# Optimization experiments

Hardware: AMD Instinct MI355X
Metric: run time of the kernel (lower is better)

## Reference

```python
import jax, jax.numpy as jnp
import numpy as np

B, S, D_MODEL, D_ATTN = 4, 2048, 1024, 1024
NEG_INF = jnp.float32(-jnp.inf)


def setup_inputs() -> dict:
    key = jax.random.key(0)
    ks = jax.random.split(key, 6)
    scale = 1.0 / np.sqrt(D_MODEL)
    return {
        "x": jax.random.normal(ks[0], (B, S, D_MODEL), dtype=jnp.float32),
        "mask": jnp.ones((B, S), dtype=jnp.float32),
        "Wq": jax.random.normal(ks[1], (D_ATTN, D_MODEL), dtype=jnp.float32) * scale,
        "Wk": jax.random.normal(ks[2], (D_ATTN, D_MODEL), dtype=jnp.float32) * scale,
        "Wv": jax.random.normal(ks[3], (D_ATTN, D_MODEL), dtype=jnp.float32) * scale,
        "Wo": jax.random.normal(ks[4], (D_MODEL, D_ATTN), dtype=jnp.float32) * scale,
        "bo": jnp.zeros((D_MODEL,), dtype=jnp.float32),
    }


def reference(x, mask, Wq, Wk, Wv, Wo, bo):
    # x: [B,S,Dm]; torch Linear weight is [out,in], so y = x @ W.T
    q = jnp.einsum("bsd,ad->bsa", x, Wq)  # [B,S,Da]
    k = jnp.einsum("bsd,ad->bsa", x, Wk)
    v = jnp.einsum("bsd,ad->bsa", x, Wv)  # NOTE: v from x (original quirk)
    logits = jnp.einsum("bqa,bka->bqk", q, k)  # [B,S,S]
    # causal mask (cross_attention=True path): keep lower triangle incl. diag
    causal = jnp.tril(jnp.ones((S, S), dtype=bool))
    logits = jnp.where(causal[None], logits, NEG_INF)
    # padding mask: outer product of per-token mask
    square_mask = mask[:, :, None] * mask[:, None, :]  # [B,S,S]
    logits = jnp.where(square_mask == 1, logits, NEG_INF)
    # scale by sqrt(d_model) AFTER masking (as in original)
    attn = jax.nn.softmax(logits / jnp.sqrt(jnp.float32(D_MODEL)), axis=-1)
    attn_out = jnp.einsum("bqk,bka->bqa", attn, v)  # [B,S,Da]
    return jnp.einsum("bsa,da->bsd", attn_out, Wo) + bo
```

## Files before the change

### kernel.cpp

```cpp
#include <hip/hip_runtime.h>
#include <hip/hip_bf16.h>
#include <cstdio>

typedef __bf16 bf16x8 __attribute__((ext_vector_type(8)));
typedef float f32x4 __attribute__((ext_vector_type(4)));

#define BM 128
#define BN 128
#define BK 64

__device__ __forceinline__ unsigned short f2bf(float f) {
  union { float f; unsigned u; } v; v.f = f;
  unsigned u = v.u;
  return (unsigned short)((u + 0x7FFFu + ((u >> 16) & 1u)) >> 16);
}

__device__ __forceinline__ float bf2f(unsigned short s) {
  union { unsigned u; float f; } v; v.u = ((unsigned)s) << 16;
  return v.f;
}

#define GLOAD16(gsrc, ldst) \
  __builtin_amdgcn_global_load_lds((const __attribute__((address_space(1))) void*)(gsrc), \
                                   (__attribute__((address_space(3))) void*)(ldst), 16, 0, 0)

#define SB_KLOOP(Ab, Bb)                                                        \
  for (int kt = 0; kt < 16; kt++) {                                             \
    const unsigned short* Ak = (Ab) + kt * BK;                                  \
    const unsigned short* Bk = (Bb) + kt * BK;                                  \
    _Pragma("unroll")                                                           \
    for (int r = 0; r < 4; r++) {                                               \
      int row = r * 32 + srow;                                                  \
      int sc = sch ^ (row & 7);                                                 \
      GLOAD16(Ak + (long)row * 1024 + sc * 8, &lds[0][(r * 32 + wave * 8) * BK]);\
    }                                                                           \
    _Pragma("unroll")                                                           \
    for (int r = 0; r < 4; r++) {                                               \
      int row = r * 32 + srow;                                                  \
      int sc = sch ^ (row & 7);                                                 \
      GLOAD16(Bk + (long)row * 1024 + sc * 8, &lds[1][(r * 32 + wave * 8) * BK]);\
    }                                                                           \
    __syncthreads();                                                            \
    _Pragma("unroll")                                                           \
    for (int s = 0; s < 2; s++) {                                               \
      bf16x8 av[4], bv[4];                                                      \
      _Pragma("unroll")                                                         \
      for (int i = 0; i < 4; i++) av[i] = *reinterpret_cast<const bf16x8*>(lds[0] + aOff[i][s]); \
      _Pragma("unroll")                                                         \
      for (int j = 0; j < 4; j++) bv[j] = *reinterpret_cast<const bf16x8*>(lds[1] + bOff[j][s]); \
      _Pragma("unroll")                                                         \
      for (int i = 0; i < 4; i++)                                               \
        _Pragma("unroll")                                                       \
        for (int j = 0; j < 4; j++)                                             \
          acc[i][j] = __builtin_amdgcn_mfma_f32_16x16x32_bf16(av[i], bv[j], acc[i][j], 0, 0, 0); \
    }                                                                           \
    __syncthreads();                                                            \
  }

#define SB_PREAMBLE                                                             \
  const int tid = threadIdx.x;                                                  \
  const int lane = tid & 63;                                                    \
  const int wave = tid >> 6;                                                    \
  const int wr = wave >> 1, wc = wave & 1;                                      \
  const int srow = tid >> 3;                                                    \
  const int sch = tid & 7;                                                      \
  const f32x4 fzero = {0.f, 0.f, 0.f, 0.f};                                     \
  f32x4 acc[4][4];                                                              \
  _Pragma("unroll")                                                             \
  for (int i = 0; i < 4; i++)                                                   \
    _Pragma("unroll")                                                           \
    for (int j = 0; j < 4; j++) acc[i][j] = fzero;                              \
  int aOff[4][2], bOff[4][2];                                                   \
  _Pragma("unroll")                                                             \
  for (int i = 0; i < 4; i++) {                                                 \
    _Pragma("unroll")                                                           \
    for (int s = 0; s < 2; s++) {                                               \
      int ra = wr * 64 + i * 16 + (lane & 15);                                  \
      aOff[i][s] = ra * BK + (((s * 4 + (lane >> 4)) ^ (ra & 7)) * 8);          \
      int rb = wc * 64 + i * 16 + (lane & 15);                                  \
      bOff[i][s] = rb * BK + (((s * 4 + (lane >> 4)) ^ (rb & 7)) * 8);          \
    }                                                                           \
  }

__global__ __launch_bounds__(256)
void cast_w(const float* __restrict__ Wq, const float* __restrict__ Wk,
            const float* __restrict__ Wv, const float* __restrict__ Wo,
            unsigned short* __restrict__ Wqk, unsigned short* __restrict__ Wob,
            unsigned short* __restrict__ Wvt)
{
  const int blk = blockIdx.x;
  const int tid = threadIdx.x;
  if (blk < 1536) {
    const int w = blk >> 9;
    const int off = blk & 511;
    const float* src = (w == 0) ? Wq : (w == 1) ? Wk : Wo;
    unsigned short* dst = (w == 0) ? Wqk : (w == 1) ? (Wqk + 1024L * 1024) : Wob;
    const int i = (off * 256 + tid) * 8;
    float4 a = *reinterpret_cast<const float4*>(src + i);
    float4 b = *reinterpret_cast<const float4*>(src + i + 4);
    union { unsigned short us[8]; uint4 u4; } pk;
    pk.us[0] = f2bf(a.x); pk.us[1] = f2bf(a.y); pk.us[2] = f2bf(a.z); pk.us[3] = f2bf(a.w);
    pk.us[4] = f2bf(b.x); pk.us[5] = f2bf(b.y); pk.us[6] = f2bf(b.z); pk.us[7] = f2bf(b.w);
    *reinterpret_cast<uint4*>(dst + i) = pk.u4;
    return;
  }
  __shared__ float t[64][65];
  const int tile = blk - 1536;
  const int a0 = (tile >> 4) * 64;
  const int m0 = (tile & 15) * 64;
#pragma unroll
  for (int i = 0; i < 4; i++) {
    const int row = (tid >> 4) + i * 16;
    const int col4 = tid & 15;
    float4 f4 = *reinterpret_cast<const float4*>(Wv + (long)(a0 + row) * 1024 + m0 + col4 * 4);
    t[row][col4 * 4 + 0] = f4.x;
    t[row][col4 * 4 + 1] = f4.y;
    t[row][col4 * 4 + 2] = f4.z;
    t[row][col4 * 4 + 3] = f4.w;
  }
  __syncthreads();
#pragma unroll
  for (int j = 0; j < 2; j++) {
    const int mm = (tid >> 3) + j * 32;
    const int aa0 = (tid & 7) * 8;
    union { unsigned short us[8]; uint4 u4; } pk;
#pragma unroll
    for (int u = 0; u < 8; u++) pk.us[u] = f2bf(t[aa0 + u][mm]);
    *reinterpret_cast<uint4*>(Wvt + (long)(m0 + mm) * 1024 + a0 + aa0) = pk.u4;
  }
}

__global__ __launch_bounds__(256, 3)
void prep2(const float* __restrict__ x, unsigned short* __restrict__ xb,
           const unsigned short* __restrict__ Wob, const unsigned short* __restrict__ Wvt,
           unsigned short* __restrict__ Wvo)
{
  __shared__ short lds[2][BM * BK];
  if (blockIdx.x >= 64) {
    const int blk = blockIdx.x - 64;
    const int i = (blk * 256 + (int)threadIdx.x) * 8;
    float4 a = *reinterpret_cast<const float4*>(x + i);
    float4 b = *reinterpret_cast<const float4*>(x + i + 4);
    union { unsigned short us[8]; uint4 u4; } pk;
    pk.us[0] = f2bf(a.x); pk.us[1] = f2bf(a.y); pk.us[2] = f2bf(a.z); pk.us[3] = f2bf(a.w);
    pk.us[4] = f2bf(b.x); pk.us[5] = f2bf(b.y); pk.us[6] = f2bf(b.z); pk.us[7] = f2bf(b.w);
    *reinterpret_cast<uint4*>(xb + i) = pk.u4;
    return;
  }
  const int t = blockIdx.x;
  const int m0 = (t >> 3) * BM, n0 = (t & 7) * BN;
  const unsigned short* Ab = Wob + (long)m0 * 1024;
  const unsigned short* Bb = Wvt + (long)n0 * 1024;

  SB_PREAMBLE
  SB_KLOOP(Ab, Bb)

  const int rb4 = (lane >> 4) * 4;
  const int cl = lane & 15;
#pragma unroll
  for (int i = 0; i < 4; i++) {
#pragma unroll
    for (int j = 0; j < 4; j++) {
      const int gm = m0 + wr * 64 + i * 16 + rb4;
      const int gn = n0 + wc * 64 + j * 16 + cl;
#pragma unroll
      for (int r = 0; r < 4; r++)
        Wvo[(long)(gm + r) * 1024 + gn] = f2bf(acc[i][j][r]);
    }
  }
}

__global__ __launch_bounds__(256, 3)
void dispA2(const unsigned short* __restrict__ Xbf, const unsigned short* __restrict__ Wqk,
            const unsigned short* __restrict__ Wvo,
            unsigned short* __restrict__ Qb, unsigned short* __restrict__ Kb,
            unsigned short* __restrict__ VWt)
{
  __shared__ short lds[2][BM * BK];
  const int flat = blockIdx.x;
  const bool isQK = flat < 1024;
  int m0, n0;
  const unsigned short *Ab, *Bb;
  if (isQK) {
    const int swz = (flat & 7) * 128 + (flat >> 3);
    const int bx = swz & 15, by = swz >> 4;
    m0 = by * BM; n0 = bx * BN;
    Ab = Xbf + (long)m0 * 1024;
    Bb = Wqk + (long)n0 * 1024;
  } else {
    const int t = flat - 1024;
    const int swz = (t & 7) * 64 + (t >> 3);
    const int bx = swz & 7, by = swz >> 3;
    m0 = by * BM; n0 = bx * BN;
    Ab = Xbf + (long)m0 * 1024;
    Bb = Wvo + (long)n0 * 1024;
  }

  SB_PREAMBLE
  SB_KLOOP(Ab, Bb)

  const int rb4 = (lane >> 4) * 4;
  const int cl = lane & 15;
#pragma unroll
  for (int i = 0; i < 4; i++) {
#pragma unroll
    for (int j = 0; j < 4; j++) {
      const int gm = m0 + wr * 64 + i * 16 + rb4;
      const int gn = n0 + wc * 64 + j * 16 + cl;
      if (isQK) {
        if (gn < 1024) {
#pragma unroll
          for (int r = 0; r < 4; r++)
            Qb[(long)(gm + r) * 1024 + gn] = f2bf(acc[i][j][r]);
        } else {
#pragma unroll
          for (int r = 0; r < 4; r++)
            Kb[(long)(gm + r) * 1024 + (gn - 1024)] = f2bf(acc[i][j][r]);
        }
      } else {
        const int b = gm >> 11;
        const int sIdx = gm & 2047;
        unsigned short* C = VWt + (long)b * (2048L * 1024) + (long)gn * 2048 + sIdx;
        ushort4 pk;
        pk.x = f2bf(acc[i][j][0]);
        pk.y = f2bf(acc[i][j][1]);
        pk.z = f2bf(acc[i][j][2]);
        pk.w = f2bf(acc[i][j][3]);
        *reinterpret_cast<ushort4*>(C) = pk;
      }
    }
  }
}

__global__ __launch_bounds__(256, 3)
void dispS(const unsigned short* __restrict__ Qb, const unsigned short* __restrict__ Kb,
           unsigned short* __restrict__ Sb)
{
  __shared__ short lds[2][BM * BK];
  const int t = blockIdx.x;
  const int bz = t / 136;
  const int tt = t - bz * 136;
  const int swz = (tt & 7) * 17 + (tt >> 3);
  int i = (int)((sqrtf(8.f * (float)swz + 1.f) - 1.f) * 0.5f);
  while ((i + 1) * (i + 2) / 2 <= swz) ++i;
  while (i * (i + 1) / 2 > swz) --i;
  const int j = swz - i * (i + 1) / 2;
  const int m0 = i * BM, n0 = j * BN;
  const unsigned short* Ab = Qb + ((long)bz * 2048 + m0) * 1024;
  const unsigned short* Bb = Kb + ((long)bz * 2048 + n0) * 1024;

  SB_PREAMBLE
  SB_KLOOP(Ab, Bb)

  const int rb4 = (lane >> 4) * 4;
  const int cl = lane & 15;
  unsigned short* C = Sb + (long)bz * (2048L * 2048);
#pragma unroll
  for (int ii = 0; ii < 4; ii++) {
#pragma unroll
    for (int jj = 0; jj < 4; jj++) {
      const int gm = m0 + wr * 64 + ii * 16 + rb4;
      const int gn = n0 + wc * 64 + jj * 16 + cl;
#pragma unroll
      for (int r = 0; r < 4; r++)
        C[(long)(gm + r) * 2048 + gn] = f2bf(acc[ii][jj][r] * 0.03125f);
    }
  }
}

__global__ __launch_bounds__(256, 2)
void gemm_pv(const unsigned short* __restrict__ A, const unsigned short* __restrict__ B,
             float* __restrict__ Cv, const float* __restrict__ bias,
             int K, int ldA, int ldB, int ldC,
             long aBat, long bBat, long cBat)
{
  const int gx = gridDim.x;
  const int nwg = gx * gridDim.y;
  const int flat = blockIdx.y * gx + blockIdx.x;
  const int qch = nwg >> 3, rch = nwg & 7;
  const int xcd = flat & 7, idx = flat >> 3;
  const int swz = (xcd < rch ? xcd * (qch + 1) : rch * (qch + 1) + (xcd - rch) * qch) + idx;
  const int bx = swz % gx;
  const int bz = blockIdx.z;
  int by = swz / gx;
  if (bz >= 2) by = gridDim.y - 1 - by;

  const int m0 = by * BM;
  const int n0 = bx * BN;

  const unsigned short* Ab = A + (long)bz * aBat + (long)m0 * ldA;
  const unsigned short* Bb = B + (long)bz * bBat + (long)n0 * ldB;

  __shared__ short lds[2][2][BM * BK];

  const int tid = threadIdx.x;
  const int lane = tid & 63;
  const int wave = tid >> 6;
  const int wr = wave >> 1, wc = wave & 1;

  const int Keff = min(K, m0 + BM);
  const int nk = Keff / BK;

  const int srow = tid >> 3;
  const int sch = tid & 7;

  const f32x4 fzero = {0.f, 0.f, 0.f, 0.f};
  f32x4 acc[4][4];
#pragma unroll
  for (int i = 0; i < 4; i++)
#pragma unroll
    for (int j = 0; j < 4; j++) acc[i][j] = fzero;

  int aOff[4][2], bOff[4][2];
#pragma unroll
  for (int i = 0; i < 4; i++) {
#pragma unroll
    for (int s = 0; s < 2; s++) {
      int ra = wr * 64 + i * 16 + (lane & 15);
      aOff[i][s] = ra * BK + (((s * 4 + (lane >> 4)) ^ (ra & 7)) * 8);
      int rb = wc * 64 + i * 16 + (lane & 15);
      bOff[i][s] = rb * BK + (((s * 4 + (lane >> 4)) ^ (rb & 7)) * 8);
    }
  }

  auto stage = [&](int buf, int kt) {
    const unsigned short* Ak = Ab + kt * BK;
    const unsigned short* Bk = Bb + kt * BK;
#pragma unroll
    for (int r = 0; r < 4; r++) {
      int row = r * 32 + srow;
      int sc = sch ^ (row & 7);
      GLOAD16(Ak + (long)row * ldA + sc * 8, &lds[buf][0][(r * 32 + wave * 8) * BK]);
    }
#pragma unroll
    for (int r = 0; r < 4; r++) {
      int row = r * 32 + srow;
      int sc = sch ^ (row & 7);
      GLOAD16(Bk + (long)row * ldB + sc * 8, &lds[buf][1][(r * 32 + wave * 8) * BK]);
    }
  };

  stage(0, 0);
  stage(1, 1);
  asm volatile("s_waitcnt vmcnt(8)" ::: "memory");
  __builtin_amdgcn_sched_barrier(0);
  __builtin_amdgcn_s_barrier();

  int cur = 0;
  for (int kt = 0; kt < nk; kt++) {
    const short* La = lds[cur][0];
    const short* Lb = lds[cur][1];
    bf16x8 av[2][4], bv[2][4];
#pragma unroll
    for (int s = 0; s < 2; s++) {
#pragma unroll
      for (int i = 0; i < 4; i++) {
        av[s][i] = *reinterpret_cast<const bf16x8*>(La + aOff[i][s]);
        bv[s][i] = *reinterpret_cast<const bf16x8*>(Lb + bOff[i][s]);
      }
    }
    asm volatile("s_waitcnt lgkmcnt(0)" ::: "memory");
    __builtin_amdgcn_sched_barrier(0);
    __builtin_amdgcn_s_barrier();
    __builtin_amdgcn_sched_barrier(0);

    if (kt + 2 < nk) {
      stage(cur, kt + 2);
      asm volatile("s_waitcnt vmcnt(8)" ::: "memory");
    } else if (kt + 1 < nk) {
      asm volatile("s_waitcnt vmcnt(0)" ::: "memory");
    }
    if (kt + 1 < nk) {
      __builtin_amdgcn_s_barrier();
      __builtin_amdgcn_sched_barrier(0);
    }

    __builtin_amdgcn_s_setprio(1);
#pragma unroll
    for (int s = 0; s < 2; s++)
#pragma unroll
      for (int i = 0; i < 4; i++)
#pragma unroll
        for (int j = 0; j < 4; j++)
          acc[i][j] = __builtin_amdgcn_mfma_f32_16x16x32_bf16(av[s][i], bv[s][j], acc[i][j], 0, 0, 0);
    __builtin_amdgcn_s_setprio(0);
    __builtin_amdgcn_sched_barrier(0);
    cur ^= 1;
  }

  const int rb4 = (lane >> 4) * 4;
  const int cl = lane & 15;
#pragma unroll
  for (int i = 0; i < 4; i++) {
#pragma unroll
    for (int j = 0; j < 4; j++) {
      const int gm = m0 + wr * 64 + i * 16 + rb4;
      const int gn = n0 + wc * 64 + j * 16 + cl;
      float* C = Cv + (long)bz * cBat;
      const float bb = bias[gn];
#pragma unroll
      for (int r = 0; r < 4; r++)
        C[(long)(gm + r) * ldC + gn] = acc[i][j][r] + bb;
    }
  }
}

__global__ __launch_bounds__(256)
void softmax_rows(const unsigned short* __restrict__ Sb, const float* __restrict__ maskv,
                  unsigned short* __restrict__ P, int Sdim)
{
  const int wv = threadIdx.x >> 6;
  const int lane = threadIdx.x & 63;
  const int q = blockIdx.x * 4 + wv;
  const int b = blockIdx.y;
  const int kmax = (q & ~127) + 128;
  const unsigned short* row = Sb + ((long)b * Sdim + q) * Sdim;
  unsigned short* prow = P + ((long)b * Sdim + q) * Sdim;
  const float* mrow = maskv + (long)b * Sdim;
  const float mq = mrow[q];

  float v[4][8];
  float mx = -INFINITY;
#pragma unroll
  for (int c = 0; c < 4; c++) {
    const int k0 = c * 512 + lane * 8;
    if (c * 512 < kmax) {
      uint4 raw = *reinterpret_cast<const uint4*>(row + k0);
      const unsigned short* us = reinterpret_cast<const unsigned short*>(&raw);
      float4 ma = *reinterpret_cast<const float4*>(mrow + k0);
      float4 mb = *reinterpret_cast<const float4*>(mrow + k0 + 4);
      float mv[8] = {ma.x, ma.y, ma.z, ma.w, mb.x, mb.y, mb.z, mb.w};
#pragma unroll
      for (int u = 0; u < 8; u++) {
        const int k = k0 + u;
        const bool ok = (k <= q) && (mq * mv[u] == 1.0f);
        v[c][u] = ok ? bf2f(us[u]) : -INFINITY;
        mx = fmaxf(mx, v[c][u]);
      }
    } else {
#pragma unroll
      for (int u = 0; u < 8; u++) v[c][u] = -INFINITY;
    }
  }
#pragma unroll
  for (int o = 32; o; o >>= 1) mx = fmaxf(mx, __shfl_xor(mx, o));

  float sm = 0.f;
#pragma unroll
  for (int c = 0; c < 4; c++)
#pragma unroll
    for (int u = 0; u < 8; u++) {
      v[c][u] = (v[c][u] > -INFINITY) ? __expf(v[c][u] - mx) : 0.f;
      sm += v[c][u];
    }
#pragma unroll
  for (int o = 32; o; o >>= 1) sm += __shfl_xor(sm, o);
  const float inv = 1.0f / sm;

#pragma unroll
  for (int c = 0; c < 4; c++) {
    if (c * 512 < kmax) {
      union { unsigned short us[8]; uint4 u4; } pk;
#pragma unroll
      for (int u = 0; u < 8; u++) pk.us[u] = f2bf(v[c][u] * inv);
      *reinterpret_cast<uint4*>(prow + c * 512 + lane * 8) = pk.u4;
    }
  }
}

extern "C" void kernel_launch(void* const* d_in, const int* in_sizes, int n_in,
                              void* d_out, int out_size, void* d_ws, size_t ws_size,
                              hipStream_t stream)
{
  const int B = 4, S = 2048, D = 1024;
  const float* x  = (const float*)d_in[0];
  const float* mk = (const float*)d_in[1];
  const float* Wq = (const float*)d_in[2];
  const float* Wk = (const float*)d_in[3];
  const float* Wv = (const float*)d_in[4];
  const float* Wo = (const float*)d_in[5];
  const float* bo = (const float*)d_in[6];
  float* out = (float*)d_out;

  char* ws = (char*)d_ws;
  const long MB = 1024L * 1024L;
  unsigned short* Xbf  = (unsigned short*)(ws + 0);
  unsigned short* Qb   = (unsigned short*)(ws + 16 * MB);
  unsigned short* Kb   = (unsigned short*)(ws + 32 * MB);
  unsigned short* VWt  = (unsigned short*)(ws + 48 * MB);
  unsigned short* Wqk  = (unsigned short*)(ws + 64 * MB);
  unsigned short* Wvo  = (unsigned short*)(ws + 68 * MB);
  unsigned short* Wob  = (unsigned short*)(ws + 70 * MB);
  unsigned short* Sbuf = (unsigned short*)(ws + 72 * MB);
  unsigned short* Wvt  = Sbuf;
  unsigned short* P    = Qb;

  if (ws_size < (size_t)(104 * MB)) {
    fprintf(stderr, "kernel_launch: ws too small (%zu bytes, need 104MB)\n", ws_size);
    return;
  }

  cast_w<<<dim3(1792), dim3(256), 0, stream>>>(Wq, Wk, Wv, Wo, Wqk, Wob, Wvt);
  prep2<<<dim3(4160), dim3(256), 0, stream>>>(x, Xbf, Wob, Wvt, Wvo);
  dispA2<<<dim3(1536), dim3(256), 0, stream>>>(Xbf, Wqk, Wvo, Qb, Kb, VWt);
  dispS<<<dim3(544), dim3(256), 0, stream>>>(Qb, Kb, Sbuf);
  softmax_rows<<<dim3(512, 4), dim3(256), 0, stream>>>(Sbuf, mk, P, 2048);
  dim3 gO(1024 / BN, 2048 / BM, 4);
  gemm_pv<<<gO, dim3(256), 0, stream>>>(P, VWt, out, bo,
                                        2048, 2048, 2048, 1024,
                                        (long)S * S, (long)D * S, (long)S * D);
}
```

Measured before the change: 155.7 us.

## Fuse weight casting and Wo·Wv product into one prep kernel

```diff
diff --git a/kernel.cpp b/kernel.cpp
--- a/kernel.cpp
+++ b/kernel.cpp
@@ -64,6 +64,7 @@
   const int wr = wave >> 1, wc = wave & 1;                                      \
   const int srow = tid >> 3;                                                    \
   const int sch = tid & 7;                                                      \
+  (void)srow; (void)sch;                                                        \
   const f32x4 fzero = {0.f, 0.f, 0.f, 0.f};                                     \
   f32x4 acc[4][4];                                                              \
   _Pragma("unroll")                                                             \
@@ -82,20 +83,30 @@
     }                                                                           \
   }
 
-__global__ __launch_bounds__(256)
-void cast_w(const float* __restrict__ Wq, const float* __restrict__ Wk,
-            const float* __restrict__ Wv, const float* __restrict__ Wo,
-            unsigned short* __restrict__ Wqk, unsigned short* __restrict__ Wob,
-            unsigned short* __restrict__ Wvt)
+__global__ __launch_bounds__(256, 3)
+void prep_all(const float* __restrict__ x, const float* __restrict__ Wq,
+              const float* __restrict__ Wk, const float* __restrict__ Wv,
+              const float* __restrict__ Wo,
+              unsigned short* __restrict__ xb, unsigned short* __restrict__ Wqk,
+              unsigned short* __restrict__ Wvo)
 {
+  __shared__ short lds[2][BM * BK];
   const int blk = blockIdx.x;
-  const int tid = threadIdx.x;
-  if (blk < 1536) {
-    const int w = blk >> 9;
-    const int off = blk & 511;
-    const float* src = (w == 0) ? Wq : (w == 1) ? Wk : Wo;
-    unsigned short* dst = (w == 0) ? Wqk : (w == 1) ? (Wqk + 1024L * 1024) : Wob;
-    const int i = (off * 256 + tid) * 8;
+
+  if (blk >= 64) {
+    const int tid = threadIdx.x;
+    const float* src;
+    unsigned short* dst;
+    int i;
+    if (blk < 4160) {
+      src = x; dst = xb; i = ((blk - 64) * 256 + tid) * 8;
+    } else {
+      const int w = (blk - 4160) >> 9;
+      const int off = (blk - 4160) & 511;
+      src = (w == 0) ? Wq : Wk;
+      dst = Wqk + (long)w * 1024 * 1024;
+      i = (off * 256 + tid) * 8;
+    }
     float4 a = *reinterpret_cast<const float4*>(src + i);
     float4 b = *reinterpret_cast<const float4*>(src + i + 4);
     union { unsigned short us[8]; uint4 u4; } pk;
@@ -104,56 +115,57 @@
     *reinterpret_cast<uint4*>(dst + i) = pk.u4;
     return;
   }
-  __shared__ float t[64][65];
-  const int tile = blk - 1536;
-  const int a0 = (tile >> 4) * 64;
-  const int m0 = (tile & 15) * 64;
-#pragma unroll
-  for (int i = 0; i < 4; i++) {
-    const int row = (tid >> 4) + i * 16;
-    const int col4 = tid & 15;
-    float4 f4 = *reinterpret_cast<const float4*>(Wv + (long)(a0 + row) * 1024 + m0 + col4 * 4);
-    t[row][col4 * 4 + 0] = f4.x;
-    t[row][col4 * 4 + 1] = f4.y;
-    t[row][col4 * 4 + 2] = f4.z;
-    t[row][col4 * 4 + 3] = f4.w;
-  }
-  __syncthreads();
-#pragma unroll
-  for (int j = 0; j < 2; j++) {
-    const int mm = (tid >> 3) + j * 32;
-    const int aa0 = (tid & 7) * 8;
-    union { unsigned short us[8]; uint4 u4; } pk;
-#pragma unroll
-    for (int u = 0; u < 8; u++) pk.us[u] = f2bf(t[aa0 + u][mm]);
-    *reinterpret_cast<uint4*>(Wvt + (long)(m0 + mm) * 1024 + a0 + aa0) = pk.u4;
-  }
-}
-
-__global__ __launch_bounds__(256, 3)
-void prep2(const float* __restrict__ x, unsigned short* __restrict__ xb,
-           const unsigned short* __restrict__ Wob, const unsigned short* __restrict__ Wvt,
-           unsigned short* __restrict__ Wvo)
-{
-  __shared__ short lds[2][BM * BK];
-  if (blockIdx.x >= 64) {
-    const int blk = blockIdx.x - 64;
-    const int i = (blk * 256 + (int)threadIdx.x) * 8;
-    float4 a = *reinterpret_cast<const float4*>(x + i);
-    float4 b = *reinterpret_cast<const float4*>(x + i + 4);
-    union { unsigned short us[8]; uint4 u4; } pk;
-    pk.us[0] = f2bf(a.x); pk.us[1] = f2bf(a.y); pk.us[2] = f2bf(a.z); pk.us[3] = f2bf(a.w);
-    pk.us[4] = f2bf(b.x); pk.us[5] = f2bf(b.y); pk.us[6] = f2bf(b.z); pk.us[7] = f2bf(b.w);
-    *reinterpret_cast<uint4*>(xb + i) = pk.u4;
-    return;
-  }
-  const int t = blockIdx.x;
-  const int m0 = (t >> 3) * BM, n0 = (t & 7) * BN;
-  const unsigned short* Ab = Wob + (long)m0 * 1024;
-  const unsigned short* Bb = Wvt + (long)n0 * 1024;
+
+  const int m0 = (blk >> 3) * BM, n0 = (blk & 7) * BN;
 
   SB_PREAMBLE
-  SB_KLOOP(Ab, Bb)
+
+  for (int kt = 0; kt < 16; kt++) {
+#pragma unroll
+    for (int p = 0; p < 4; p++) {
+      const int row = p * 32 + (tid >> 3);
+      const int oct = tid & 7;
+      const float* src = Wo + (long)(m0 + row) * 1024 + kt * 64 + oct * 8;
+      float4 a = *reinterpret_cast<const float4*>(src);
+      float4 b = *reinterpret_cast<const float4*>(src + 4);
+      union { unsigned short us[8]; uint4 u4; } pk;
+      pk.us[0] = f2bf(a.x); pk.us[1] = f2bf(a.y); pk.us[2] = f2bf(a.z); pk.us[3] = f2bf(a.w);
+      pk.us[4] = f2bf(b.x); pk.us[5] = f2bf(b.y); pk.us[6] = f2bf(b.z); pk.us[7] = f2bf(b.w);
+      *reinterpret_cast<uint4*>(&lds[0][row * 64 + ((oct ^ (row & 7)) * 8)]) = pk.u4;
+    }
+    {
+      const int kl = tid >> 2;
+      const int nq = tid & 3;
+      const float* src = Wv + (long)(kt * 64 + kl) * 1024 + n0 + nq * 32;
+      const int swz_base = ((kl >> 3) * 8) + (kl & 7);
+#pragma unroll
+      for (int j = 0; j < 8; j++) {
+        float4 f = *reinterpret_cast<const float4*>(src + j * 4);
+        float vv[4] = {f.x, f.y, f.z, f.w};
+#pragma unroll
+        for (int u = 0; u < 4; u++) {
+          const int n = nq * 32 + j * 4 + u;
+          lds[1][n * 64 + (((kl >> 3) ^ (n & 7)) * 8) + (kl & 7)] = (short)f2bf(vv[u]);
+        }
+      }
+      (void)swz_base;
+    }
+    __syncthreads();
+#pragma unroll
+    for (int s = 0; s < 2; s++) {
+      bf16x8 av[4], bv[4];
+#pragma unroll
+      for (int i = 0; i < 4; i++) av[i] = *reinterpret_cast<const bf16x8*>(lds[0] + aOff[i][s]);
+#pragma unroll
+      for (int j = 0; j < 4; j++) bv[j] = *reinterpret_cast<const bf16x8*>(lds[1] + bOff[j][s]);
+#pragma unroll
+      for (int i = 0; i < 4; i++)
+#pragma unroll
+        for (int j = 0; j < 4; j++)
+          acc[i][j] = __builtin_amdgcn_mfma_f32_16x16x32_bf16(av[i], bv[j], acc[i][j], 0, 0, 0);
+    }
+    __syncthreads();
+  }
 
   const int rb4 = (lane >> 4) * 4;
   const int cl = lane & 15;
@@ -490,9 +502,7 @@
   unsigned short* VWt  = (unsigned short*)(ws + 48 * MB);
   unsigned short* Wqk  = (unsigned short*)(ws + 64 * MB);
   unsigned short* Wvo  = (unsigned short*)(ws + 68 * MB);
-  unsigned short* Wob  = (unsigned short*)(ws + 70 * MB);
   unsigned short* Sbuf = (unsigned short*)(ws + 72 * MB);
-  unsigned short* Wvt  = Sbuf;
   unsigned short* P    = Qb;
 
   if (ws_size < (size_t)(104 * MB)) {
@@ -500,8 +510,7 @@
     return;
   }
 
-  cast_w<<<dim3(1792), dim3(256), 0, stream>>>(Wq, Wk, Wv, Wo, Wqk, Wob, Wvt);
-  prep2<<<dim3(4160), dim3(256), 0, stream>>>(x, Xbf, Wob, Wvt, Wvo);
+  prep_all<<<dim3(5184), dim3(256), 0, stream>>>(x, Wq, Wk, Wv, Wo, Xbf, Wqk, Wvo);
   dispA2<<<dim3(1536), dim3(256), 0, stream>>>(Xbf, Wqk, Wvo, Qb, Kb, VWt);
   dispS<<<dim3(544), dim3(256), 0, stream>>>(Qb, Kb, Sbuf);
   softmax_rows<<<dim3(512, 4), dim3(256), 0, stream>>>(Sbuf, mk, P, 2048);
```

Result: slower. 186.4 us (+19.7%).
